# Optimization experiments

Measured on AMD Instinct MI355X. Metric: run time of the kernel, lower is better.

## Reference

```python
import jax, jax.numpy as jnp
import numpy as np

N_NODES = 2048
N_EDGES = 32768
N_GRAPH = 64
D_INJ = 240
D_EMB = 480
D_FEAT = 512
H = 4
DH = 120
SH_DIM = 9
N_RBF = 128
CUTOFF = 5.0
AVG_DEGREE = 16.0
AVG_NUM_NODES = 32.0
N_ITER = 2
MAX_ATOM = 64


def _ln(x):
    mu = jnp.mean(x, axis=-1, keepdims=True)
    var = jnp.var(x, axis=-1, keepdims=True)
    return (x - mu) * jax.lax.rsqrt(var + 1e-6)


def _sph(u):
    # component-normalized real spherical harmonics l=0,1,2 of unit vectors u [E,3]
    x, y, z = u[:, 0], u[:, 1], u[:, 2]
    s3 = np.sqrt(3.0); s15 = np.sqrt(15.0); s5 = np.sqrt(5.0)
    return jnp.stack([
        jnp.ones_like(x),
        s3 * x, s3 * y, s3 * z,
        s15 * x * y, s15 * y * z,
        0.5 * s5 * (3.0 * z * z - 1.0),
        s15 * x * z, 0.5 * s15 * (x * x - y * y)], axis=-1)


def _block(z, esrc, edst, sh, rbf, Wq, Wk, Wv, Wsh, Wr, Wo, F1, F2, res_ffn):
    # equivariant-style dot-product attention: gather -> edge compute -> segment softmax -> scatter
    x = _ln(z)
    q = (x @ Wq)[edst].reshape(-1, H, DH)
    k = (x @ Wk)[esrc].reshape(-1, H, DH)
    v = (x @ Wv)[esrc].reshape(-1, H, DH)
    m = (sh @ Wsh).reshape(-1, H, DH)          # SH tensor-product message modulation
    r = jax.nn.silu(rbf @ Wr)[:, :, None]      # radial gate per head [E,H,1]
    k = (k + m) * r
    v = (v + m) * r
    logit = jnp.sum(q * k, axis=-1) / np.sqrt(DH)   # [E,H]
    mx = jax.ops.segment_max(logit, edst, num_segments=N_NODES)
    mx = jnp.where(jnp.isfinite(mx), mx, 0.0)
    ex = jnp.exp(logit - mx[edst])
    den = jax.ops.segment_sum(ex, edst, num_segments=N_NODES)
    alpha = ex / (den[edst] + 1e-9)
    agg = jax.ops.segment_sum(alpha[:, :, None] * v, edst, num_segments=N_NODES)
    y = z + agg.reshape(N_NODES, H * DH) @ Wo
    out = jax.nn.silu(_ln(y) @ F1) @ F2
    return y + out if res_ffn else out


def _forward(pos, atom_table, degWr, degWsh,
             b0_Wq, b0_Wk, b0_Wv, b0_Wsh, b0_Wr, b0_Wo, b0_F1, b0_F2,
             bm_Wq, bm_Wk, bm_Wv, bm_Wsh, bm_Wr, bm_Wo, bm_F1, bm_F2,
             bf_Wq, bf_Wk, bf_Wv, bf_Wsh, bf_Wr, bf_Wo, bf_F1, bf_F2,
             hW1, hW2, node_atom, edge_src, edge_dst, batch):
    # ---- encode ----
    vec = pos[edge_src] - pos[edge_dst]
    d = jnp.sqrt(jnp.sum(vec * vec, axis=-1) + 1e-12)
    sh = _sph(vec / d[:, None])                              # [E,9]
    centers = jnp.linspace(0.0, CUTOFF, N_RBF)
    width = CUTOFF / N_RBF
    rbf = jnp.exp(-0.5 * jnp.square((d[:, None] - centers) / width))  # [E,128]
    atom = atom_table[node_atom]                             # [N,240]
    rad = jax.nn.silu(rbf @ degWr)                           # [E,9]
    deg = jax.ops.segment_sum((sh * rad) @ degWsh, edge_dst, num_segments=N_NODES) / AVG_DEGREE
    inj = atom + deg                                         # input-injection features
    # ---- DEQ fixed-point (unrolled) ----
    z = jnp.zeros((N_NODES, D_EMB), dtype=pos.dtype)
    for _ in range(N_ITER):
        z = _block(jnp.concatenate([z, inj], axis=-1), edge_src, edge_dst, sh, rbf,
                   b0_Wq, b0_Wk, b0_Wv, b0_Wsh, b0_Wr, b0_Wo, b0_F1, b0_F2, False)
        for i in range(4):
            z = _block(z, edge_src, edge_dst, sh, rbf,
                       bm_Wq[i], bm_Wk[i], bm_Wv[i], bm_Wsh[i], bm_Wr[i],
                       bm_Wo[i], bm_F1[i], bm_F2[i], True)
    # ---- decode ----
    feat = _block(z, edge_src, edge_dst, sh, rbf,
                  bf_Wq, bf_Wk, bf_Wv, bf_Wsh, bf_Wr, bf_Wo, bf_F1, bf_F2, False)
    feat = _ln(feat)
    e_node = jax.nn.silu(feat @ hW1) @ hW2                   # [N,1]
    return jax.ops.segment_sum(e_node, batch, num_segments=N_GRAPH) / np.sqrt(AVG_NUM_NODES)


def setup_inputs() -> dict:
    key = jax.random.key(0)
    it = iter(jax.random.split(key, 40))
    def nrm(shape):
        fan = shape[-2] if len(shape) >= 2 else shape[-1]
        return jax.random.normal(next(it), shape, jnp.float32) / np.sqrt(fan)
    inp = {}
    inp['pos'] = jax.random.normal(next(it), (N_NODES, 3), jnp.float32) * 2.0
    inp['node_atom'] = jax.random.randint(next(it), (N_NODES,), 0, MAX_ATOM)
    inp['edge_src'] = jax.random.randint(next(it), (N_EDGES,), 0, N_NODES)
    inp['edge_dst'] = jax.random.randint(next(it), (N_EDGES,), 0, N_NODES)
    inp['batch'] = jnp.sort(jax.random.randint(next(it), (N_NODES,), 0, N_GRAPH))
    inp['atom_table'] = nrm((MAX_ATOM, D_INJ))
    inp['degWr'] = nrm((N_RBF, SH_DIM))
    inp['degWsh'] = nrm((SH_DIM, D_INJ))
    DZ = D_EMB + D_INJ
    inp['b0_Wq'] = nrm((DZ, H * DH)); inp['b0_Wk'] = nrm((DZ, H * DH)); inp['b0_Wv'] = nrm((DZ, H * DH))
    inp['b0_Wsh'] = nrm((SH_DIM, H * DH)); inp['b0_Wr'] = nrm((N_RBF, H))
    inp['b0_Wo'] = nrm((H * DH, DZ)); inp['b0_F1'] = nrm((DZ, D_EMB)); inp['b0_F2'] = nrm((D_EMB, D_EMB))
    inp['bm_Wq'] = nrm((4, D_EMB, H * DH)); inp['bm_Wk'] = nrm((4, D_EMB, H * DH)); inp['bm_Wv'] = nrm((4, D_EMB, H * DH))
    inp['bm_Wsh'] = nrm((4, SH_DIM, H * DH)); inp['bm_Wr'] = nrm((4, N_RBF, H))
    inp['bm_Wo'] = nrm((4, H * DH, D_EMB)); inp['bm_F1'] = nrm((4, D_EMB, D_EMB)); inp['bm_F2'] = nrm((4, D_EMB, D_EMB))
    inp['bf_Wq'] = nrm((D_EMB, H * DH)); inp['bf_Wk'] = nrm((D_EMB, H * DH)); inp['bf_Wv'] = nrm((D_EMB, H * DH))
    inp['bf_Wsh'] = nrm((SH_DIM, H * DH)); inp['bf_Wr'] = nrm((N_RBF, H))
    inp['bf_Wo'] = nrm((H * DH, D_EMB)); inp['bf_F1'] = nrm((D_EMB, D_EMB)); inp['bf_F2'] = nrm((D_EMB, D_FEAT))
    inp['hW1'] = nrm((D_FEAT, D_FEAT)); inp['hW2'] = nrm((D_FEAT, 1))
    return inp


def reference(pos, atom_table, degWr, degWsh,
              b0_Wq, b0_Wk, b0_Wv, b0_Wsh, b0_Wr, b0_Wo, b0_F1, b0_F2,
              bm_Wq, bm_Wk, bm_Wv, bm_Wsh, bm_Wr, bm_Wo, bm_F1, bm_F2,
              bf_Wq, bf_Wk, bf_Wv, bf_Wsh, bf_Wr, bf_Wo, bf_F1, bf_F2,
              hW1, hW2, node_atom, edge_src, edge_dst, batch):
    return _forward(pos, atom_table, degWr, degWsh,
                    b0_Wq, b0_Wk, b0_Wv, b0_Wsh, b0_Wr, b0_Wo, b0_F1, b0_F2,
                    bm_Wq, bm_Wk, bm_Wv, bm_Wsh, bm_Wr, bm_Wo, bm_F1, bm_F2,
                    bf_Wq, bf_Wk, bf_Wv, bf_Wsh, bf_Wr, bf_Wo, bf_F1, bf_F2,
                    hW1, hW2, node_atom, edge_src, edge_dst, batch)
```

## Files before the change

### kernel.cpp

```cpp
#include <hip/hip_runtime.h>

#define NN 2048
#define NE 32768
#define NG 64
#define DINJ 240
#define DEMB 480
#define DFEAT 512
#define MAXDEG 192

typedef unsigned short ushort_t;
typedef __attribute__((ext_vector_type(8))) short short8;
typedef __attribute__((ext_vector_type(4))) float floatx4;

__device__ __forceinline__ float b2f(ushort_t u){
  union { unsigned u; float f; } x; x.u = ((unsigned)u) << 16; return x.f;
}
__device__ __forceinline__ ushort_t f2b(float f){
  union { float f; unsigned u; } x; x.f = f;
  unsigned r = x.u + 0x7FFFu + ((x.u >> 16) & 1u);
  return (ushort_t)(r >> 16);
}
__device__ __forceinline__ float wredsum(float v){
  #pragma unroll
  for (int o = 32; o > 0; o >>= 1) v += __shfl_xor(v, o, 64);
  return v;
}
__device__ __forceinline__ float silu_f(float x){ return x / (1.f + __expf(-x)); }

__global__ void zero_f32(float* p, int n){
  int i = blockIdx.x*256 + threadIdx.x; if (i < n) p[i] = 0.f;
}

__global__ void detect_kernel(const ushort_t* __restrict__ probe, int* flag){
  __shared__ int c;
  if (threadIdx.x == 0) c = 0;
  __syncthreads();
  ushort_t u = probe[2*threadIdx.x];
  int e = (u >> 7) & 0xFF;
  int plausible = (u == 0) || (e >= 100 && e <= 140);
  atomicAdd(&c, plausible);
  __syncthreads();
  if (threadIdx.x == 0) *flag = (c >= 192) ? 0 : 1;
}

struct CDesc { const void* src; float* dst; int n; };
struct CDescArr { CDesc d[11]; };
__global__ __launch_bounds__(256) void convert_inputs(CDescArr ca, const int* __restrict__ flag){
  CDesc cd = ca.d[blockIdx.y];
  int isf32 = *flag;
  for (int i = blockIdx.x*256 + threadIdx.x; i < cd.n; i += gridDim.x*256){
    cd.dst[i] = isf32 ? ((const float*)cd.src)[i] : b2f(((const ushort_t*)cd.src)[i]);
  }
}

struct TDesc { const void* src; ushort_t* dh; ushort_t* dl; int K; int M; int Kpad; int Mpad; int eoff; };
struct TDescArr { TDesc d[37]; };
__global__ __launch_bounds__(256) void transpose_all(TDescArr ta, const int* __restrict__ flag){
  TDesc td = ta.d[blockIdx.z];
  int k0 = blockIdx.x*32, m0 = blockIdx.y*32;
  if (k0 >= td.Kpad || m0 >= td.Mpad) return;
  int isf32 = *flag;
  __shared__ float lds[32*33];
  int tx = threadIdx.x & 31, ty = threadIdx.x >> 5;
  #pragma unroll
  for (int r = 0; r < 4; ++r){
    int kl = ty + r*8;
    int k = k0 + kl, mm = m0 + tx;
    float x = 0.f;
    if (k < td.K && mm < td.M){
      size_t si = (size_t)td.eoff + (size_t)k*td.M + mm;
      x = isf32 ? ((const float*)td.src)[si] : b2f(((const ushort_t*)td.src)[si]);
    }
    lds[kl*33 + tx] = x;
  }
  __syncthreads();
  #pragma unroll
  for (int r = 0; r < 4; ++r){
    int nl = ty + r*8;
    int n = m0 + nl, k = k0 + tx;
    if (n < td.Mpad && k < td.Kpad){
      float x = lds[tx*33 + nl];
      ushort_t h = f2b(x);
      size_t di = (size_t)n*td.Kpad + k;
      td.dh[di] = h;
      td.dl[di] = f2b(x - b2f(h));
    }
  }
}

__global__ void pack_wr(const float* __restrict__ b0Wr, const float* __restrict__ bmWr,
                        const float* __restrict__ bfWr, float* __restrict__ Wr_all){
  int idx = blockIdx.x*256 + threadIdx.x; if (idx >= 128*24) return;
  int k = idx / 24, o = idx - k*24;
  int slot = o >> 2, h = o & 3;
  const float* Wr = (slot == 0) ? b0Wr : ((slot <= 4) ? bmWr + (size_t)(slot-1)*512 : bfWr);
  Wr_all[idx] = Wr[k*4+h];
}

__global__ __launch_bounds__(128) void edge_all_kernel(
    const float* __restrict__ pos,
    const int* __restrict__ esrc, const int* __restrict__ edst,
    const float* __restrict__ degWr, const float* __restrict__ Wr_all,
    float* __restrict__ sh_out, float* __restrict__ t9,
    float* __restrict__ r_all){
  __shared__ float w9L[128*9];
  __shared__ float w24L[128*24];
  int t = threadIdx.x;
  for (int i = t; i < 128*9; i += 128)  w9L[i]  = degWr[i];
  for (int i = t; i < 128*24; i += 128) w24L[i] = Wr_all[i];
  __syncthreads();
  int e = blockIdx.x*128 + t; if (e >= NE) return;
  int s = esrc[e], d = edst[e];
  float x = pos[s*3+0] - pos[d*3+0];
  float y = pos[s*3+1] - pos[d*3+1];
  float z = pos[s*3+2] - pos[d*3+2];
  float dd = sqrtf(x*x + y*y + z*z + 1e-12f);
  float ix = x/dd, iy = y/dd, iz = z/dd;
  const float s3 = 1.7320508075688772f, s15 = 3.872983346207417f, s5 = 2.23606797749979f;
  float sh[9];
  sh[0] = 1.f; sh[1] = s3*ix; sh[2] = s3*iy; sh[3] = s3*iz;
  sh[4] = s15*ix*iy; sh[5] = s15*iy*iz; sh[6] = 0.5f*s5*(3.f*iz*iz - 1.f);
  sh[7] = s15*ix*iz; sh[8] = 0.5f*s15*(ix*ix - iy*iy);
  #pragma unroll
  for (int j = 0; j < 9; ++j) sh_out[(size_t)e*9+j] = sh[j];
  float t9a[9], ga[24];
  #pragma unroll
  for (int j = 0; j < 9; ++j) t9a[j] = 0.f;
  #pragma unroll
  for (int o = 0; o < 24; ++o) ga[o] = 0.f;
  for (int k = 0; k < 128; ++k){
    float c = (float)k * (5.0f/127.0f);
    float u = (dd - c) * (128.0f/5.0f);
    float rb = __expf(-0.5f*u*u);
    const float* w9  = w9L + k*9;
    const float* w24 = w24L + k*24;
    #pragma unroll
    for (int j = 0; j < 9; ++j) t9a[j] += rb*w9[j];
    #pragma unroll
    for (int o = 0; o < 24; ++o) ga[o] += rb*w24[o];
  }
  #pragma unroll
  for (int j = 0; j < 9; ++j) t9[(size_t)e*9+j] = sh[j]*silu_f(t9a[j]);
  #pragma unroll
  for (int o = 0; o < 24; ++o){
    int slot = o >> 2, h = o & 3;
    r_all[((size_t)slot*NE + e)*4 + h] = silu_f(ga[o]);
  }
}

__global__ void hist_kernel(const int* __restrict__ edst, int* counts){
  int e = blockIdx.x*256 + threadIdx.x; if (e < NE) atomicAdd(&counts[edst[e]], 1);
}
__global__ __launch_bounds__(1024) void scan_kernel(const int* __restrict__ counts,
                                                    int* rowptr, int* cursor){
  __shared__ int s[1024];
  int t = threadIdx.x;
  int c0 = counts[2*t], c1 = counts[2*t+1];
  s[t] = c0 + c1;
  __syncthreads();
  for (int off = 1; off < 1024; off <<= 1){
    int v = (t >= off) ? s[t-off] : 0;
    __syncthreads();
    s[t] += v;
    __syncthreads();
  }
  int excl = s[t] - (c0 + c1);
  rowptr[2*t]   = excl;       cursor[2*t]   = excl;
  rowptr[2*t+1] = excl + c0;  cursor[2*t+1] = excl + c0;
  if (t == 1023) rowptr[2048] = s[1023];
}
__global__ void scatter_kernel(const int* __restrict__ edst, int* cursor, int* perm){
  int e = blockIdx.x*256 + threadIdx.x; if (e >= NE) return;
  int p = atomicAdd(&cursor[edst[e]], 1);
  perm[p] = e;
}

__global__ __launch_bounds__(64) void inj_kernel(const float* __restrict__ t9,
    const int* __restrict__ rowptr, const int* __restrict__ perm,
    const int* __restrict__ node_atom, const float* __restrict__ atom_table,
    const float* __restrict__ degWsh, float* __restrict__ inj){
  int i = blockIdx.x; int lane = threadIdx.x;
  int b = rowptr[i], e = rowptr[i+1];
  float T[9];
  #pragma unroll
  for (int j = 0; j < 9; ++j) T[j] = 0.f;
  for (int idx = b; idx < e; ++idx){
    int ed = perm[idx];
    #pragma unroll
    for (int j = 0; j < 9; ++j) T[j] += t9[(size_t)ed*9+j];
  }
  int a = node_atom[i];
  for (int c = lane; c < DINJ; c += 64){
    float s = 0.f;
    #pragma unroll
    for (int j = 0; j < 9; ++j) s += T[j]*degWsh[j*DINJ+c];
    inj[(size_t)i*DINJ+c] = atom_table[(size_t)a*DINJ+c] + s*(1.0f/16.0f);
  }
}

__global__ __launch_bounds__(256) void ln_kernel(const float* __restrict__ in, int D,
                                                 int Kpad, ushort_t* __restrict__ oh){
  int i = blockIdx.x*4 + (threadIdx.x >> 6);
  int lane = threadIdx.x & 63;
  const float* row = in + (size_t)i*D;
  float s = 0.f, sq = 0.f;
  for (int d = lane; d < D; d += 64){ float x = row[d]; s += x; sq += x*x; }
  s = wredsum(s); sq = wredsum(sq);
  float mu = s / (float)D;
  float var = fmaxf(sq / (float)D - mu*mu, 0.f);
  float rs = rsqrtf(var + 1e-6f);
  ushort_t* ohrow = oh + (size_t)i*Kpad;
  for (int d = lane; d < D; d += 64) ohrow[d] = f2b((row[d]-mu)*rs);
  for (int d = D + lane; d < Kpad; d += 64) ohrow[d] = 0;
}

__global__ __launch_bounds__(256) void ln_cat_kernel(const float* __restrict__ z,
    const float* __restrict__ inj, ushort_t* __restrict__ oh){
  int i = blockIdx.x*4 + (threadIdx.x >> 6);
  int lane = threadIdx.x & 63;
  const float* zr = z + (size_t)i*480;
  const float* ir = inj + (size_t)i*240;
  float s = 0.f, sq = 0.f;
  for (int d = lane; d < 720; d += 64){
    float x = (d < 480) ? zr[d] : ir[d-480];
    s += x; sq += x*x;
  }
  s = wredsum(s); sq = wredsum(sq);
  float mu = s * (1.0f/720.0f);
  float var = fmaxf(sq * (1.0f/720.0f) - mu*mu, 0.f);
  float rs = rsqrtf(var + 1e-6f);
  ushort_t* ohrow = oh + (size_t)i*736;
  for (int d = lane; d < 720; d += 64){
    float x = (d < 480) ? zr[d] : ir[d-480];
    ohrow[d] = f2b((x-mu)*rs);
  }
  for (int d = 720 + lane; d < 736; d += 64) ohrow[d] = 0;
}

template<int KPAD, bool SPLITB>
__global__ __launch_bounds__(256) void gemm_bt(
    const ushort_t* __restrict__ A,
    const ushort_t* __restrict__ BTh, const ushort_t* __restrict__ BTl,
    int N, int ldc,
    float* __restrict__ Cf, ushort_t* __restrict__ Cb,
    const float* __restrict__ R, const float* __restrict__ R2, int flags){
  int lane = threadIdx.x & 63, wave = threadIdx.x >> 6;
  int row0 = blockIdx.y*64 + (wave>>1)*32;
  int col0 = blockIdx.x*64 + (wave&1)*32;
  int m = lane & 15, q4 = lane >> 4;
  size_t a0 = (size_t)(row0+m)*KPAD + q4*8;
  size_t a1 = a0 + (size_t)16*KPAD;
  size_t b0 = (size_t)(col0+m)*KPAD + q4*8;
  size_t b1 = b0 + (size_t)16*KPAD;
  floatx4 acc00 = {0,0,0,0}, acc01 = {0,0,0,0}, acc10 = {0,0,0,0}, acc11 = {0,0,0,0};
  constexpr int steps = KPAD >> 5;
  constexpr int DEPTH = SPLITB ? 3 : 4;
  struct Frag { short8 A0, A1, B0h, B1h, B0l, B1l; };
  auto loadF = [&](int s) -> Frag {
    Frag f;
    size_t o = (size_t)s*32;
    f.A0  = *(const short8*)(A   + a0 + o);
    f.A1  = *(const short8*)(A   + a1 + o);
    f.B0h = *(const short8*)(BTh + b0 + o);
    f.B1h = *(const short8*)(BTh + b1 + o);
    if (SPLITB){
      f.B0l = *(const short8*)(BTl + b0 + o);
      f.B1l = *(const short8*)(BTl + b1 + o);
    }
    return f;
  };
  Frag ring[DEPTH];
  #pragma unroll
  for (int d = 0; d < DEPTH; ++d) ring[d] = loadF(d < steps ? d : steps-1);
  #pragma unroll
  for (int s = 0; s < steps; ++s){
    Frag cur = ring[s % DEPTH];
    if (s + DEPTH < steps) ring[s % DEPTH] = loadF(s + DEPTH);
    acc00 = __builtin_amdgcn_mfma_f32_16x16x32_bf16(cur.A0, cur.B0h, acc00, 0, 0, 0);
    acc01 = __builtin_amdgcn_mfma_f32_16x16x32_bf16(cur.A0, cur.B1h, acc01, 0, 0, 0);
    acc10 = __builtin_amdgcn_mfma_f32_16x16x32_bf16(cur.A1, cur.B0h, acc10, 0, 0, 0);
    acc11 = __builtin_amdgcn_mfma_f32_16x16x32_bf16(cur.A1, cur.B1h, acc11, 0, 0, 0);
    if (SPLITB){
      acc00 = __builtin_amdgcn_mfma_f32_16x16x32_bf16(cur.A0, cur.B0l, acc00, 0, 0, 0);
      acc01 = __builtin_amdgcn_mfma_f32_16x16x32_bf16(cur.A0, cur.B1l, acc01, 0, 0, 0);
      acc10 = __builtin_amdgcn_mfma_f32_16x16x32_bf16(cur.A1, cur.B0l, acc10, 0, 0, 0);
      acc11 = __builtin_amdgcn_mfma_f32_16x16x32_bf16(cur.A1, cur.B1l, acc11, 0, 0, 0);
    }
  }
  #pragma unroll
  for (int rr = 0; rr < 2; ++rr){
    #pragma unroll
    for (int cc = 0; cc < 2; ++cc){
      int col = col0 + cc*16 + m;
      if (col >= N) continue;
      floatx4 acc = rr ? (cc ? acc11 : acc10) : (cc ? acc01 : acc00);
      int rowb = row0 + rr*16 + q4*4;
      #pragma unroll
      for (int r = 0; r < 4; ++r){
        int row = rowb + r;
        size_t idx = (size_t)row*ldc + col;
        float v = acc[r];
        if (flags & 2){
          if (flags & 8)
            v += (col < 480) ? R[(size_t)row*480 + col] : R2[(size_t)row*240 + (col-480)];
          else
            v += R[idx];
        }
        if (flags & 1) v = silu_f(v);
        if (flags & 4) Cb[idx] = f2b(v);
        else           Cf[idx] = v;
      }
    }
  }
}

__global__ __launch_bounds__(256) void node_attn_kernel(
    const float* __restrict__ qkv, const float* __restrict__ sh,
    const float* __restrict__ Wsh, const float* __restrict__ r_slot,
    const int* __restrict__ rowptr, const int* __restrict__ perm,
    const int* __restrict__ esrc, ushort_t* __restrict__ aggh){
  int i = blockIdx.x; int t = threadIdx.x;
  int lane = t & 63, w = t >> 6;
  int b = rowptr[i]; int deg = min(rowptr[i+1] - b, MAXDEG);
  __shared__ float qL[480];
  __shared__ float PqL[36];
  __shared__ float logitL[MAXDEG*4];
  __shared__ float rL[MAXDEG*4];
  __shared__ int eL[MAXDEG], srcL[MAXDEG];
  __shared__ float S[36];
  __shared__ float mxs[4], dens[4];
  for (int d = t; d < 480; d += 256) qL[d] = qkv[(size_t)i*1440 + d];
  for (int idx = t; idx < deg; idx += 256){
    int e = perm[b+idx];
    eL[idx] = e;
    srcL[idx] = esrc[e];
  }
  __syncthreads();
  if (t < 36){
    int h = t/9, j = t - h*9;
    const float* ws = Wsh + (size_t)j*DEMB + h*120;
    const float* qh = qL + h*120;
    float p = 0.f;
    for (int k = 0; k < 120; ++k) p += qh[k]*ws[k];
    PqL[t] = p;
  }
  __syncthreads();
  const float inv = 0.091287092917527686f;
  for (int base = 0; base < deg; base += 64){
    int idx = base + (t >> 2);
    if (idx < deg){
      int h = t & 3;
      int e = eL[idx], s = srcL[idx];
      const float4* kk = (const float4*)(qkv + (size_t)s*1440 + 480 + h*120);
      const float4* qq = (const float4*)(qL + h*120);
      float p = 0.f;
      #pragma unroll
      for (int it = 0; it < 30; ++it){
        float4 a = qq[it], bb = kk[it];
        p += a.x*bb.x + a.y*bb.y + a.z*bb.z + a.w*bb.w;
      }
      float mmq = 0.f;
      const float* she = sh + (size_t)e*9;
      #pragma unroll
      for (int j = 0; j < 9; ++j) mmq += she[j]*PqL[h*9+j];
      float rr = r_slot[(size_t)e*4+h];
      rL[idx*4+h] = rr;
      logitL[idx*4+h] = rr*(p + mmq)*inv;
    }
  }
  __syncthreads();
  float mx = -1e30f;
  for (int idx = lane; idx < deg; idx += 64) mx = fmaxf(mx, logitL[idx*4+w]);
  #pragma unroll
  for (int o = 32; o > 0; o >>= 1) mx = fmaxf(mx, __shfl_xor(mx, o, 64));
  if (deg == 0) mx = 0.f;
  float den = 0.f;
  for (int idx = lane; idx < deg; idx += 64) den += __expf(logitL[idx*4+w]-mx);
  den = wredsum(den) + 1e-9f;
  if (lane == 0){ mxs[w] = mx; dens[w] = den; }
  __syncthreads();
  for (int j = t; j < deg*4; j += 256){
    int h = j & 3;
    logitL[j] = __expf(logitL[j]-mxs[h]) / dens[h] * rL[j];
  }
  __syncthreads();
  float a0 = 0.f, a1 = 0.f;
  int d0 = 2*t, h2 = d0/120;
  if (t >= 240){
    for (int o = t - 240; o < 36; o += 16){
      int h = o/9, j = o - h*9;
      float a = 0.f;
      for (int idx = 0; idx < deg; ++idx)
        a += logitL[idx*4+h]*sh[(size_t)eL[idx]*9+j];
      S[o] = a;
    }
  } else {
    for (int idx = 0; idx < deg; ++idx){
      float wgt = logitL[idx*4+h2];
      float2 vv = *(const float2*)(qkv + (size_t)srcL[idx]*1440 + 960 + d0);
      a0 += wgt*vv.x; a1 += wgt*vv.y;
    }
  }
  __syncthreads();
  if (t < 240){
    float mm0 = 0.f, mm1 = 0.f;
    #pragma unroll
    for (int j = 0; j < 9; ++j){
      mm0 += S[h2*9+j]*Wsh[j*DEMB + d0];
      mm1 += S[h2*9+j]*Wsh[j*DEMB + d0 + 1];
    }
    aggh[(size_t)i*DEMB + d0]     = f2b(a0 + mm0);
    aggh[(size_t)i*DEMB + d0 + 1] = f2b(a1 + mm1);
  }
}

__global__ __launch_bounds__(256) void head_dot_kernel(const ushort_t* __restrict__ g1h,
    const float* __restrict__ hW2, const int* __restrict__ batch, float* gsum){
  int i = blockIdx.x*4 + (threadIdx.x >> 6);
  int lane = threadIdx.x & 63;
  float s = 0.f;
  for (int d = lane; d < DFEAT; d += 64)
    s += b2f(g1h[(size_t)i*DFEAT + d]) * hW2[d];
  s = wredsum(s);
  if (lane == 0) atomicAdd(&gsum[batch[i]], s);
}
__global__ void finalize_kernel(const float* __restrict__ gsum,
                                const int* __restrict__ flag, void* out){
  int g = threadIdx.x;
  if (g < NG){
    float v = gsum[g] * 0.17677669529663687f;
    if (*flag) ((float*)out)[g] = v;
    else       ((ushort_t*)out)[g] = f2b(v);
  }
}

extern "C" void kernel_launch(void* const* d_in, const int* in_sizes, int n_in,
                              void* d_out, int out_size, void* d_ws, size_t ws_size,
                              hipStream_t stream) {
  (void)in_sizes; (void)n_in; (void)out_size; (void)ws_size;
  const void* pos        = d_in[0];
  const int*  node_atom  = (const int*)d_in[1];
  const int*  esrc       = (const int*)d_in[2];
  const int*  edst       = (const int*)d_in[3];
  const int*  batch      = (const int*)d_in[4];
  const void* atom_table = d_in[5];
  const void* degWr      = d_in[6];
  const void* degWsh     = d_in[7];
  const void* b0_Wq  = d_in[8];
  const void* b0_Wk  = d_in[9];
  const void* b0_Wv  = d_in[10];
  const void* b0_Wsh = d_in[11];
  const void* b0_Wr  = d_in[12];
  const void* b0_Wo  = d_in[13];
  const void* b0_F1  = d_in[14];
  const void* b0_F2  = d_in[15];
  const void* bm_Wq  = d_in[16];
  const void* bm_Wk  = d_in[17];
  const void* bm_Wv  = d_in[18];
  const void* bm_Wsh = d_in[19];
  const void* bm_Wr  = d_in[20];
  const void* bm_Wo  = d_in[21];
  const void* bm_F1  = d_in[22];
  const void* bm_F2  = d_in[23];
  const void* bf_Wq  = d_in[24];
  const void* bf_Wk  = d_in[25];
  const void* bf_Wv  = d_in[26];
  const void* bf_Wsh = d_in[27];
  const void* bf_Wr  = d_in[28];
  const void* bf_Wo  = d_in[29];
  const void* bf_F1  = d_in[30];
  const void* bf_F2  = d_in[31];
  const void* hW1    = d_in[32];
  const void* hW2    = d_in[33];

  char* bws = (char*)d_ws;
  size_t off = 0;
  auto alloc = [&](size_t bytes) -> void* {
    void* p = bws + off;
    off += (bytes + 255) & ~(size_t)255;
    return p;
  };
  int* dflag   = (int*)alloc(256);
  float* sh_f  = (float*)alloc((size_t)NE*9*4);
  float* t9    = (float*)alloc((size_t)NE*9*4);
  int* counts  = (int*)alloc(2048*4);
  int* rowptr  = (int*)alloc(2049*4);
  int* cursor  = (int*)alloc(2048*4);
  int* perm    = (int*)alloc((size_t)NE*4);
  float* injb  = (float*)alloc((size_t)NN*DINJ*4);
  float* zA    = (float*)alloc((size_t)NN*512*4);
  float* zB    = (float*)alloc((size_t)NN*512*4);
  ushort_t* xlnh = (ushort_t*)alloc((size_t)NN*736*2);
  float* qkvb  = (float*)alloc((size_t)NN*1440*4);
  float* Wr_all = (float*)alloc((size_t)128*24*4);
  float* r_all = (float*)alloc((size_t)6*NE*4*4);
  ushort_t* aggh = (ushort_t*)alloc((size_t)NN*DEMB*2);
  float* ybuf  = (float*)alloc((size_t)NN*720*4);
  ushort_t* h1h = (ushort_t*)alloc((size_t)NN*DEMB*2);
  ushort_t* g1h = (ushort_t*)alloc((size_t)NN*DFEAT*2);
  float* gsum  = (float*)alloc(64*4);

  float* pos_c    = (float*)alloc((size_t)NN*3*4);
  float* atom_c   = (float*)alloc((size_t)64*DINJ*4);
  float* degWr_c  = (float*)alloc((size_t)128*9*4);
  float* degWsh_c = (float*)alloc((size_t)9*DINJ*4);
  float* b0_Wsh_c = (float*)alloc((size_t)9*480*4);
  float* b0_Wr_c  = (float*)alloc((size_t)128*4*4);
  float* bm_Wsh_c = (float*)alloc((size_t)4*9*480*4);
  float* bm_Wr_c  = (float*)alloc((size_t)4*128*4*4);
  float* bf_Wsh_c = (float*)alloc((size_t)9*480*4);
  float* bf_Wr_c  = (float*)alloc((size_t)128*4*4);
  float* hW2_c    = (float*)alloc((size_t)512*4);

  auto allocW = [&](size_t elems, ushort_t*& h, ushort_t*& l){
    h = (ushort_t*)alloc(elems*2); l = (ushort_t*)alloc(elems*2);
  };
  ushort_t *b0_qkvTh,*b0_qkvTl,*b0_WoTh,*b0_WoTl,*b0_F1Th,*b0_F1Tl,*b0_F2Th,*b0_F2Tl;
  allocW((size_t)1472*736, b0_qkvTh, b0_qkvTl);
  allocW((size_t)768*480,  b0_WoTh,  b0_WoTl);
  allocW((size_t)512*736,  b0_F1Th,  b0_F1Tl);
  allocW((size_t)512*480,  b0_F2Th,  b0_F2Tl);
  ushort_t *bm_qkvTh[4],*bm_qkvTl[4],*bm_WoTh[4],*bm_WoTl[4],*bm_F1Th[4],*bm_F1Tl[4],*bm_F2Th[4],*bm_F2Tl[4];
  for (int i = 0; i < 4; ++i){
    allocW((size_t)1472*480, bm_qkvTh[i], bm_qkvTl[i]);
    allocW((size_t)512*480,  bm_WoTh[i],  bm_WoTl[i]);
    allocW((size_t)512*480,  bm_F1Th[i],  bm_F1Tl[i]);
    allocW((size_t)512*480,  bm_F2Th[i],  bm_F2Tl[i]);
  }
  ushort_t *bf_qkvTh,*bf_qkvTl,*bf_WoTh,*bf_WoTl,*bf_F1Th,*bf_F1Tl,*bf_F2Th,*bf_F2Tl,*hW1Th,*hW1Tl;
  allocW((size_t)1472*480, bf_qkvTh, bf_qkvTl);
  allocW((size_t)512*480,  bf_WoTh,  bf_WoTl);
  allocW((size_t)512*480,  bf_F1Th,  bf_F1Tl);
  allocW((size_t)512*480,  bf_F2Th,  bf_F2Tl);
  allocW((size_t)512*512,  hW1Th,    hW1Tl);

  detect_kernel<<<1, 256, 0, stream>>>((const ushort_t*)atom_table, dflag);

  CDescArr ca;
  int ci = 0;
  auto addC = [&](const void* s, float* d, int n){
    ca.d[ci].src = s; ca.d[ci].dst = d; ca.d[ci].n = n; ++ci;
  };
  addC(pos, pos_c, NN*3);
  addC(atom_table, atom_c, 64*DINJ);
  addC(degWr, degWr_c, 128*9);
  addC(degWsh, degWsh_c, 9*DINJ);
  addC(b0_Wsh, b0_Wsh_c, 9*480);
  addC(b0_Wr, b0_Wr_c, 128*4);
  addC(bm_Wsh, bm_Wsh_c, 4*9*480);
  addC(bm_Wr, bm_Wr_c, 4*128*4);
  addC(bf_Wsh, bf_Wsh_c, 9*480);
  addC(bf_Wr, bf_Wr_c, 128*4);
  addC(hW2, hW2_c, 512);
  convert_inputs<<<dim3(8, 11), 256, 0, stream>>>(ca, dflag);

  TDescArr ta;
  int ti = 0;
  auto addT = [&](const void* s, ushort_t* dh, ushort_t* dl, int K, int M,
                  int Kp, int Mp, int rowoff, int eo){
    ta.d[ti].src = s;
    ta.d[ti].dh = dh + (size_t)rowoff*Kp;
    ta.d[ti].dl = dl + (size_t)rowoff*Kp;
    ta.d[ti].K = K; ta.d[ti].M = M; ta.d[ti].Kpad = Kp; ta.d[ti].Mpad = Mp;
    ta.d[ti].eoff = eo; ++ti;
  };
  addT(b0_Wq, b0_qkvTh, b0_qkvTl, 720, 480, 736, 480, 0,   0);
  addT(b0_Wk, b0_qkvTh, b0_qkvTl, 720, 480, 736, 480, 480, 0);
  addT(b0_Wv, b0_qkvTh, b0_qkvTl, 720, 480, 736, 512, 960, 0);
  addT(b0_Wo, b0_WoTh,  b0_WoTl,  480, 720, 480, 768, 0,   0);
  addT(b0_F1, b0_F1Th,  b0_F1Tl,  720, 480, 736, 512, 0,   0);
  addT(b0_F2, b0_F2Th,  b0_F2Tl,  480, 480, 480, 512, 0,   0);
  for (int i = 0; i < 4; ++i){
    int eo = i*480*480;
    addT(bm_Wq, bm_qkvTh[i], bm_qkvTl[i], 480, 480, 480, 480, 0,   eo);
    addT(bm_Wk, bm_qkvTh[i], bm_qkvTl[i], 480, 480, 480, 480, 480, eo);
    addT(bm_Wv, bm_qkvTh[i], bm_qkvTl[i], 480, 480, 480, 512, 960, eo);
    addT(bm_Wo, bm_WoTh[i],  bm_WoTl[i],  480, 480, 480, 512, 0,   eo);
    addT(bm_F1, bm_F1Th[i],  bm_F1Tl[i],  480, 480, 480, 512, 0,   eo);
    addT(bm_F2, bm_F2Th[i],  bm_F2Tl[i],  480, 480, 480, 512, 0,   eo);
  }
  addT(bf_Wq, bf_qkvTh, bf_qkvTl, 480, 480, 480, 480, 0,   0);
  addT(bf_Wk, bf_qkvTh, bf_qkvTl, 480, 480, 480, 480, 480, 0);
  addT(bf_Wv, bf_qkvTh, bf_qkvTl, 480, 480, 480, 512, 960, 0);
  addT(bf_Wo, bf_WoTh,  bf_WoTl,  480, 480, 480, 512, 0,   0);
  addT(bf_F1, bf_F1Th,  bf_F1Tl,  480, 480, 480, 512, 0,   0);
  addT(bf_F2, bf_F2Th,  bf_F2Tl,  480, 512, 480, 512, 0,   0);
  addT(hW1,   hW1Th,    hW1Tl,    512, 512, 512, 512, 0,   0);
  transpose_all<<<dim3(23, 24, 37), 256, 0, stream>>>(ta, dflag);

  pack_wr<<<12, 256, 0, stream>>>(b0_Wr_c, bm_Wr_c, bf_Wr_c, Wr_all);
  edge_all_kernel<<<NE/128, 128, 0, stream>>>(pos_c, esrc, edst, degWr_c, Wr_all,
                                              sh_f, t9, r_all);

  zero_f32<<<(2048 + 255)/256, 256, 0, stream>>>((float*)counts, 2048);
  hist_kernel<<<NE/256, 256, 0, stream>>>(edst, counts);
  scan_kernel<<<1, 1024, 0, stream>>>(counts, rowptr, cursor);
  scatter_kernel<<<NE/256, 256, 0, stream>>>(edst, cursor, perm);

  inj_kernel<<<NN, 64, 0, stream>>>(t9, rowptr, perm, node_atom, atom_c, degWsh_c, injb);
  zero_f32<<<(NN*DEMB)/256, 256, 0, stream>>>(zA, NN*DEMB);

  auto gemm = [&](const ushort_t* A, const ushort_t* BTh, const ushort_t* BTl,
                  int N, int Npad, int Kp, int ldc,
                  float* Cf, ushort_t* Cb, const float* R, const float* R2,
                  int flags, bool split){
    dim3 g(Npad/64, 32);
    if (split){
      if (Kp == 480)
        gemm_bt<480,true><<<g, 256, 0, stream>>>(A, BTh, BTl, N, ldc, Cf, Cb, R, R2, flags);
      else if (Kp == 512)
        gemm_bt<512,true><<<g, 256, 0, stream>>>(A, BTh, BTl, N, ldc, Cf, Cb, R, R2, flags);
      else
        gemm_bt<736,true><<<g, 256, 0, stream>>>(A, BTh, BTl, N, ldc, Cf, Cb, R, R2, flags);
    } else {
      if (Kp == 480)
        gemm_bt<480,false><<<g, 256, 0, stream>>>(A, BTh, BTl, N, ldc, Cf, Cb, R, R2, flags);
      else if (Kp == 512)
        gemm_bt<512,false><<<g, 256, 0, stream>>>(A, BTh, BTl, N, ldc, Cf, Cb, R, R2, flags);
      else
        gemm_bt<736,false><<<g, 256, 0, stream>>>(A, BTh, BTl, N, ldc, Cf, Cb, R, R2, flags);
    }
  };

  struct BW {
    const float *Wsh, *r_slot;
    const ushort_t *qkvTh,*qkvTl,*WoTh,*WoTl,*F1Th,*F1Tl,*F2Th,*F2Tl;
    int Din, Kpad, Dout; bool res;
  };
  auto run_block = [&](const BW& bw, const float* zin, const float* zinj, float* zout){
    if (zinj) ln_cat_kernel<<<NN/4, 256, 0, stream>>>(zin, zinj, xlnh);
    else      ln_kernel<<<NN/4, 256, 0, stream>>>(zin, bw.Din, bw.Kpad, xlnh);
    gemm(xlnh, bw.qkvTh, bw.qkvTl, 1440, 1472, bw.Kpad, 1440,
         qkvb, nullptr, nullptr, nullptr, 0, true);
    node_attn_kernel<<<NN, 256, 0, stream>>>(qkvb, sh_f, bw.Wsh, bw.r_slot,
                                             rowptr, perm, esrc, aggh);
    int WoNpad = (bw.Din == 720) ? 768 : 512;
    gemm(aggh, bw.WoTh, bw.WoTl, bw.Din, WoNpad, 480, bw.Din,
         ybuf, nullptr, zin, zinj, zinj ? (2|8) : 2, false);
    ln_kernel<<<NN/4, 256, 0, stream>>>(ybuf, bw.Din, bw.Kpad, xlnh);
    gemm(xlnh, bw.F1Th, bw.F1Tl, DEMB, 512, bw.Kpad, DEMB,
         nullptr, h1h, nullptr, nullptr, 1|4, false);
    gemm(h1h, bw.F2Th, bw.F2Tl, bw.Dout, 512, 480, bw.Dout,
         zout, nullptr, bw.res ? ybuf : nullptr, nullptr, bw.res ? 2 : 0, false);
  };

  BW b0 = { b0_Wsh_c, r_all + (size_t)0*NE*4,
            b0_qkvTh,b0_qkvTl,b0_WoTh,b0_WoTl,b0_F1Th,b0_F1Tl,b0_F2Th,b0_F2Tl,
            720, 736, 480, false };
  BW bm[4];
  for (int i = 0; i < 4; ++i){
    bm[i] = { bm_Wsh_c + (size_t)i*9*480, r_all + (size_t)(1+i)*NE*4,
              bm_qkvTh[i],bm_qkvTl[i],bm_WoTh[i],bm_WoTl[i],
              bm_F1Th[i],bm_F1Tl[i],bm_F2Th[i],bm_F2Tl[i],
              480, 480, 480, true };
  }
  BW bf = { bf_Wsh_c, r_all + (size_t)5*NE*4,
            bf_qkvTh,bf_qkvTl,bf_WoTh,bf_WoTl,bf_F1Th,bf_F1Tl,bf_F2Th,bf_F2Tl,
            480, 480, 512, false };

  float* z  = zA;
  float* z2 = zB;
  for (int iter = 0; iter < 2; ++iter){
    run_block(b0, z, injb, z2);
    { float* tmp = z; z = z2; z2 = tmp; }
    for (int i = 0; i < 4; ++i){
      run_block(bm[i], z, nullptr, z2);
      { float* tmp = z; z = z2; z2 = tmp; }
    }
  }
  run_block(bf, z, nullptr, z2);
  ln_kernel<<<NN/4, 256, 0, stream>>>(z2, DFEAT, DFEAT, xlnh);
  gemm(xlnh, hW1Th, hW1Tl, DFEAT, 512, DFEAT, DFEAT,
       nullptr, g1h, nullptr, nullptr, 1|4, true);
  zero_f32<<<1, 64, 0, stream>>>(gsum, 64);
  head_dot_kernel<<<NN/4, 256, 0, stream>>>(g1h, hW2_c, batch, gsum);
  finalize_kernel<<<1, 64, 0, stream>>>(gsum, dflag, d_out);
}
```

Baseline: 1.393 ms.

## Fuse LayerNorm into GEMM prologue using per-row stats emitted by producer GEMM epilogues

Removes the standalone LayerNorm kernels. Producer GEMMs (Wo, F2) now write per-row partial sums and sums of squares into a stats buffer from their epilogue, and inj_kernel does the same for the injection features. Consumer GEMMs read fp32 activations, rebuild mean and variance from these partials, and normalise and pack to bf16 on the fly while loading A fragments. This saves a kernel launch and a bf16 round-trip per LayerNorm. In exchange the A loads are fp32 with extra ALU work, the stats use the less stable one-pass variance, and the bf16 packing now truncates instead of rounding.

```diff
diff --git a/kernel.cpp b/kernel.cpp
--- a/kernel.cpp
+++ b/kernel.cpp
@@ -19,6 +19,9 @@
   union { float f; unsigned u; } x; x.f = f;
   unsigned r = x.u + 0x7FFFu + ((x.u >> 16) & 1u);
   return (ushort_t)(r >> 16);
+}
+__device__ __forceinline__ unsigned pk2(float a, float b){
+  return (__float_as_uint(a) >> 16) | (__float_as_uint(b) & 0xFFFF0000u);
 }
 __device__ __forceinline__ float wredsum(float v){
   #pragma unroll
@@ -178,7 +181,8 @@
 __global__ __launch_bounds__(64) void inj_kernel(const float* __restrict__ t9,
     const int* __restrict__ rowptr, const int* __restrict__ perm,
     const int* __restrict__ node_atom, const float* __restrict__ atom_table,
-    const float* __restrict__ degWsh, float* __restrict__ inj){
+    const float* __restrict__ degWsh, float* __restrict__ inj,
+    float* __restrict__ injS){
   int i = blockIdx.x; int lane = threadIdx.x;
   int b = rowptr[i], e = rowptr[i+1];
   float T[9];
@@ -190,68 +194,113 @@
     for (int j = 0; j < 9; ++j) T[j] += t9[(size_t)ed*9+j];
   }
   int a = node_atom[i];
+  float ps = 0.f, pq = 0.f;
   for (int c = lane; c < DINJ; c += 64){
     float s = 0.f;
     #pragma unroll
     for (int j = 0; j < 9; ++j) s += T[j]*degWsh[j*DINJ+c];
-    inj[(size_t)i*DINJ+c] = atom_table[(size_t)a*DINJ+c] + s*(1.0f/16.0f);
-  }
-}
-
-__global__ __launch_bounds__(256) void ln_kernel(const float* __restrict__ in, int D,
-                                                 int Kpad, ushort_t* __restrict__ oh){
-  int i = blockIdx.x*4 + (threadIdx.x >> 6);
-  int lane = threadIdx.x & 63;
-  const float* row = in + (size_t)i*D;
-  float s = 0.f, sq = 0.f;
-  for (int d = lane; d < D; d += 64){ float x = row[d]; s += x; sq += x*x; }
-  s = wredsum(s); sq = wredsum(sq);
-  float mu = s / (float)D;
-  float var = fmaxf(sq / (float)D - mu*mu, 0.f);
-  float rs = rsqrtf(var + 1e-6f);
-  ushort_t* ohrow = oh + (size_t)i*Kpad;
-  for (int d = lane; d < D; d += 64) ohrow[d] = f2b((row[d]-mu)*rs);
-  for (int d = D + lane; d < Kpad; d += 64) ohrow[d] = 0;
-}
-
-__global__ __launch_bounds__(256) void ln_cat_kernel(const float* __restrict__ z,
-    const float* __restrict__ inj, ushort_t* __restrict__ oh){
-  int i = blockIdx.x*4 + (threadIdx.x >> 6);
-  int lane = threadIdx.x & 63;
-  const float* zr = z + (size_t)i*480;
-  const float* ir = inj + (size_t)i*240;
-  float s = 0.f, sq = 0.f;
-  for (int d = lane; d < 720; d += 64){
-    float x = (d < 480) ? zr[d] : ir[d-480];
-    s += x; sq += x*x;
-  }
-  s = wredsum(s); sq = wredsum(sq);
-  float mu = s * (1.0f/720.0f);
-  float var = fmaxf(sq * (1.0f/720.0f) - mu*mu, 0.f);
-  float rs = rsqrtf(var + 1e-6f);
-  ushort_t* ohrow = oh + (size_t)i*736;
-  for (int d = lane; d < 720; d += 64){
-    float x = (d < 480) ? zr[d] : ir[d-480];
-    ohrow[d] = f2b((x-mu)*rs);
-  }
-  for (int d = 720 + lane; d < 736; d += 64) ohrow[d] = 0;
-}
-
-template<int KPAD, bool SPLITB>
+    float v = atom_table[(size_t)a*DINJ+c] + s*(1.0f/16.0f);
+    inj[(size_t)i*DINJ+c] = v;
+    ps += v; pq += v*v;
+  }
+  ps = wredsum(ps); pq = wredsum(pq);
+  if (lane == 0){ injS[i*2] = ps; injS[i*2+1] = pq; }
+}
+
+template<int KPAD, bool SPLITB, int LNA, bool STATS>
 __global__ __launch_bounds__(256) void gemm_bt(
-    const ushort_t* __restrict__ A,
+    const void* __restrict__ Abuf, const float* __restrict__ Ainj,
+    const float* __restrict__ injS,
+    const float* __restrict__ stIn, int stInStride, int nslots, int Din,
     const ushort_t* __restrict__ BTh, const ushort_t* __restrict__ BTl,
     int N, int ldc,
     float* __restrict__ Cf, ushort_t* __restrict__ Cb,
-    const float* __restrict__ R, const float* __restrict__ R2, int flags){
+    const float* __restrict__ R, const float* __restrict__ R2,
+    float* __restrict__ stOut, int stOutStride, int flags){
   int lane = threadIdx.x & 63, wave = threadIdx.x >> 6;
   int row0 = blockIdx.y*64 + (wave>>1)*32;
   int col0 = blockIdx.x*64 + (wave&1)*32;
   int m = lane & 15, q4 = lane >> 4;
-  size_t a0 = (size_t)(row0+m)*KPAD + q4*8;
-  size_t a1 = a0 + (size_t)16*KPAD;
   size_t b0 = (size_t)(col0+m)*KPAD + q4*8;
   size_t b1 = b0 + (size_t)16*KPAD;
+  int r0 = row0 + m, r1 = row0 + 16 + m;
+  const ushort_t* A16 = (const ushort_t*)Abuf;
+  const float*    A32 = (const float*)Abuf;
+  size_t a0 = 0, a1 = 0;
+  const float *az0 = nullptr, *az1 = nullptr, *aj0 = nullptr, *aj1 = nullptr;
+  float rs0 = 0.f, nm0 = 0.f, rs1 = 0.f, nm1 = 0.f;
+  if constexpr (LNA == 0){
+    a0 = (size_t)r0*KPAD + q4*8;
+    a1 = (size_t)r1*KPAD + q4*8;
+  } else {
+    int zw = (LNA == 2) ? 480 : Din;
+    az0 = A32 + (size_t)r0*zw;
+    az1 = A32 + (size_t)r1*zw;
+    if constexpr (LNA == 2){
+      aj0 = Ainj + (size_t)r0*240;
+      aj1 = Ainj + (size_t)r1*240;
+    }
+    float DD = (LNA == 2) ? 720.f : (float)Din;
+    #pragma unroll
+    for (int which = 0; which < 2; ++which){
+      int row = which ? r1 : r0;
+      float s = 0.f, q = 0.f;
+      const float* st = stIn + (size_t)row*stInStride;
+      for (int t2 = 0; t2 < nslots; ++t2){ s += st[2*t2]; q += st[2*t2+1]; }
+      if constexpr (LNA == 2){ s += injS[row*2]; q += injS[row*2+1]; }
+      float mu = s / DD;
+      float var = fmaxf(q / DD - mu*mu, 0.f);
+      float rs = rsqrtf(var + 1e-6f);
+      float nm = -mu*rs;
+      if (which){ rs1 = rs; nm1 = nm; } else { rs0 = rs; nm0 = nm; }
+    }
+  }
+  auto loadAfrag = [&](int s, int which) -> short8 {
+    if constexpr (LNA == 0){
+      size_t base = which ? a1 : a0;
+      return *(const short8*)(A16 + base + (size_t)s*32);
+    } else {
+      int k = q4*8 + s*32;
+      float x[8];
+      const float* az = which ? az1 : az0;
+      bool zero = false;
+      if constexpr (LNA == 1){
+        if (k < Din){
+          float4 p = *(const float4*)(az + k);
+          float4 q2 = *(const float4*)(az + k + 4);
+          x[0]=p.x; x[1]=p.y; x[2]=p.z; x[3]=p.w;
+          x[4]=q2.x; x[5]=q2.y; x[6]=q2.z; x[7]=q2.w;
+        } else zero = true;
+      } else {
+        if (k < 480){
+          float4 p = *(const float4*)(az + k);
+          float4 q2 = *(const float4*)(az + k + 4);
+          x[0]=p.x; x[1]=p.y; x[2]=p.z; x[3]=p.w;
+          x[4]=q2.x; x[5]=q2.y; x[6]=q2.z; x[7]=q2.w;
+        } else if (k < 720){
+          const float* aj = which ? aj1 : aj0;
+          float4 p = *(const float4*)(aj + (k - 480));
+          float4 q2 = *(const float4*)(aj + (k - 480) + 4);
+          x[0]=p.x; x[1]=p.y; x[2]=p.z; x[3]=p.w;
+          x[4]=q2.x; x[5]=q2.y; x[6]=q2.z; x[7]=q2.w;
+        } else zero = true;
+      }
+      union { short8 v; unsigned u[4]; } o;
+      if (zero){
+        o.u[0] = o.u[1] = o.u[2] = o.u[3] = 0u;
+      } else {
+        float rs = which ? rs1 : rs0;
+        float nm = which ? nm1 : nm0;
+        #pragma unroll
+        for (int p2 = 0; p2 < 4; ++p2){
+          float f0 = fmaf(x[2*p2],   rs, nm);
+          float f1 = fmaf(x[2*p2+1], rs, nm);
+          o.u[p2] = pk2(f0, f1);
+        }
+      }
+      return o.v;
+    }
+  };
   floatx4 acc00 = {0,0,0,0}, acc01 = {0,0,0,0}, acc10 = {0,0,0,0}, acc11 = {0,0,0,0};
   constexpr int steps = KPAD >> 5;
   constexpr int DEPTH = SPLITB ? 3 : 4;
@@ -259,8 +308,8 @@
   auto loadF = [&](int s) -> Frag {
     Frag f;
     size_t o = (size_t)s*32;
-    f.A0  = *(const short8*)(A   + a0 + o);
-    f.A1  = *(const short8*)(A   + a1 + o);
+    f.A0  = loadAfrag(s, 0);
+    f.A1  = loadAfrag(s, 1);
     f.B0h = *(const short8*)(BTh + b0 + o);
     f.B1h = *(const short8*)(BTh + b1 + o);
     if (SPLITB){
@@ -287,28 +336,54 @@
       acc11 = __builtin_amdgcn_mfma_f32_16x16x32_bf16(cur.A1, cur.B1l, acc11, 0, 0, 0);
     }
   }
+  float vf[2][2][4];
   #pragma unroll
   for (int rr = 0; rr < 2; ++rr){
     #pragma unroll
     for (int cc = 0; cc < 2; ++cc){
       int col = col0 + cc*16 + m;
-      if (col >= N) continue;
+      bool cv = (col < N);
       floatx4 acc = rr ? (cc ? acc11 : acc10) : (cc ? acc01 : acc00);
       int rowb = row0 + rr*16 + q4*4;
       #pragma unroll
       for (int r = 0; r < 4; ++r){
-        int row = rowb + r;
-        size_t idx = (size_t)row*ldc + col;
-        float v = acc[r];
-        if (flags & 2){
-          if (flags & 8)
-            v += (col < 480) ? R[(size_t)row*480 + col] : R2[(size_t)row*240 + (col-480)];
-          else
-            v += R[idx];
+        float v = 0.f;
+        if (cv){
+          int row = rowb + r;
+          size_t idx = (size_t)row*ldc + col;
+          v = acc[r];
+          if (flags & 2){
+            if (flags & 8)
+              v += (col < 480) ? R[(size_t)row*480 + col] : R2[(size_t)row*240 + (col-480)];
+            else
+              v += R[idx];
+          }
+          if (flags & 1) v = silu_f(v);
+          if (flags & 4) Cb[idx] = f2b(v);
+          else           Cf[idx] = v;
         }
-        if (flags & 1) v = silu_f(v);
-        if (flags & 4) Cb[idx] = f2b(v);
-        else           Cf[idx] = v;
+        vf[rr][cc][r] = v;
+      }
+    }
+  }
+  if constexpr (STATS){
+    int slot = blockIdx.x*2 + (wave & 1);
+    #pragma unroll
+    for (int rr = 0; rr < 2; ++rr){
+      #pragma unroll
+      for (int r = 0; r < 4; ++r){
+        float sm = vf[rr][0][r] + vf[rr][1][r];
+        float sq = vf[rr][0][r]*vf[rr][0][r] + vf[rr][1][r]*vf[rr][1][r];
+        #pragma unroll
+        for (int o2 = 1; o2 < 16; o2 <<= 1){
+          sm += __shfl_xor(sm, o2, 64);
+          sq += __shfl_xor(sq, o2, 64);
+        }
+        if (m == 0){
+          int row = row0 + rr*16 + q4*4 + r;
+          stOut[(size_t)row*stOutStride + slot*2]     = sm;
+          stOut[(size_t)row*stOutStride + slot*2 + 1] = sq;
+        }
       }
     }
   }
@@ -488,9 +563,12 @@
   int* cursor  = (int*)alloc(2048*4);
   int* perm    = (int*)alloc((size_t)NE*4);
   float* injb  = (float*)alloc((size_t)NN*DINJ*4);
+  float* injS  = (float*)alloc((size_t)NN*2*4);
   float* zA    = (float*)alloc((size_t)NN*512*4);
+  float* stZA  = (float*)alloc((size_t)NN*32*4);
   float* zB    = (float*)alloc((size_t)NN*512*4);
-  ushort_t* xlnh = (ushort_t*)alloc((size_t)NN*736*2);
+  float* stZB  = (float*)alloc((size_t)NN*32*4);
+  float* stY   = (float*)alloc((size_t)NN*48*4);
   float* qkvb  = (float*)alloc((size_t)NN*1440*4);
   float* Wr_all = (float*)alloc((size_t)128*24*4);
   float* r_all = (float*)alloc((size_t)6*NE*4*4);
@@ -597,81 +675,81 @@
   scan_kernel<<<1, 1024, 0, stream>>>(counts, rowptr, cursor);
   scatter_kernel<<<NE/256, 256, 0, stream>>>(edst, cursor, perm);
 
-  inj_kernel<<<NN, 64, 0, stream>>>(t9, rowptr, perm, node_atom, atom_c, degWsh_c, injb);
-  zero_f32<<<(NN*DEMB)/256, 256, 0, stream>>>(zA, NN*DEMB);
-
-  auto gemm = [&](const ushort_t* A, const ushort_t* BTh, const ushort_t* BTl,
-                  int N, int Npad, int Kp, int ldc,
-                  float* Cf, ushort_t* Cb, const float* R, const float* R2,
-                  int flags, bool split){
-    dim3 g(Npad/64, 32);
-    if (split){
-      if (Kp == 480)
-        gemm_bt<480,true><<<g, 256, 0, stream>>>(A, BTh, BTl, N, ldc, Cf, Cb, R, R2, flags);
-      else if (Kp == 512)
-        gemm_bt<512,true><<<g, 256, 0, stream>>>(A, BTh, BTl, N, ldc, Cf, Cb, R, R2, flags);
-      else
-        gemm_bt<736,true><<<g, 256, 0, stream>>>(A, BTh, BTl, N, ldc, Cf, Cb, R, R2, flags);
-    } else {
-      if (Kp == 480)
-        gemm_bt<480,false><<<g, 256, 0, stream>>>(A, BTh, BTl, N, ldc, Cf, Cb, R, R2, flags);
-      else if (Kp == 512)
-        gemm_bt<512,false><<<g, 256, 0, stream>>>(A, BTh, BTl, N, ldc, Cf, Cb, R, R2, flags);
-      else
-        gemm_bt<736,false><<<g, 256, 0, stream>>>(A, BTh, BTl, N, ldc, Cf, Cb, R, R2, flags);
-    }
-  };
+  inj_kernel<<<NN, 64, 0, stream>>>(t9, rowptr, perm, node_atom, atom_c, degWsh_c,
+                                    injb, injS);
+  zero_f32<<<(NN*544 + 255)/256, 256, 0, stream>>>(zA, NN*544);
 
   struct BW {
     const float *Wsh, *r_slot;
     const ushort_t *qkvTh,*qkvTl,*WoTh,*WoTl,*F1Th,*F1Tl,*F2Th,*F2Tl;
-    int Din, Kpad, Dout; bool res;
+    int Din, Dout; bool res;
   };
-  auto run_block = [&](const BW& bw, const float* zin, const float* zinj, float* zout){
-    if (zinj) ln_cat_kernel<<<NN/4, 256, 0, stream>>>(zin, zinj, xlnh);
-    else      ln_kernel<<<NN/4, 256, 0, stream>>>(zin, bw.Din, bw.Kpad, xlnh);
-    gemm(xlnh, bw.qkvTh, bw.qkvTl, 1440, 1472, bw.Kpad, 1440,
-         qkvb, nullptr, nullptr, nullptr, 0, true);
+  auto run_block = [&](const BW& bw, const float* zin, float* zinStats,
+                       const float* zinj, float* zout, float* zoutStats){
+    if (zinj){
+      gemm_bt<736,true,2,false><<<dim3(23,32), 256, 0, stream>>>(
+        zin, zinj, injS, zinStats, 32, 16, 720,
+        bw.qkvTh, bw.qkvTl, 1440, 1440, qkvb, nullptr,
+        nullptr, nullptr, nullptr, 0, 0);
+    } else {
+      gemm_bt<480,true,1,false><<<dim3(23,32), 256, 0, stream>>>(
+        zin, nullptr, nullptr, zinStats, 32, 16, 480,
+        bw.qkvTh, bw.qkvTl, 1440, 1440, qkvb, nullptr,
+        nullptr, nullptr, nullptr, 0, 0);
+    }
     node_attn_kernel<<<NN, 256, 0, stream>>>(qkvb, sh_f, bw.Wsh, bw.r_slot,
                                              rowptr, perm, esrc, aggh);
     int WoNpad = (bw.Din == 720) ? 768 : 512;
-    gemm(aggh, bw.WoTh, bw.WoTl, bw.Din, WoNpad, 480, bw.Din,
-         ybuf, nullptr, zin, zinj, zinj ? (2|8) : 2, false);
-    ln_kernel<<<NN/4, 256, 0, stream>>>(ybuf, bw.Din, bw.Kpad, xlnh);
-    gemm(xlnh, bw.F1Th, bw.F1Tl, DEMB, 512, bw.Kpad, DEMB,
-         nullptr, h1h, nullptr, nullptr, 1|4, false);
-    gemm(h1h, bw.F2Th, bw.F2Tl, bw.Dout, 512, 480, bw.Dout,
-         zout, nullptr, bw.res ? ybuf : nullptr, nullptr, bw.res ? 2 : 0, false);
+    gemm_bt<480,false,0,true><<<dim3(WoNpad/64,32), 256, 0, stream>>>(
+      aggh, nullptr, nullptr, nullptr, 0, 0, 0,
+      bw.WoTh, bw.WoTl, bw.Din, bw.Din, ybuf, nullptr,
+      zin, zinj, stY, 48, zinj ? (2|8) : 2);
+    if (bw.Din == 720){
+      gemm_bt<736,false,1,false><<<dim3(8,32), 256, 0, stream>>>(
+        ybuf, nullptr, nullptr, stY, 48, 24, 720,
+        bw.F1Th, bw.F1Tl, 480, 480, nullptr, h1h,
+        nullptr, nullptr, nullptr, 0, 1|4);
+    } else {
+      gemm_bt<480,false,1,false><<<dim3(8,32), 256, 0, stream>>>(
+        ybuf, nullptr, nullptr, stY, 48, 16, 480,
+        bw.F1Th, bw.F1Tl, 480, 480, nullptr, h1h,
+        nullptr, nullptr, nullptr, 0, 1|4);
+    }
+    gemm_bt<480,false,0,true><<<dim3(8,32), 256, 0, stream>>>(
+      h1h, nullptr, nullptr, nullptr, 0, 0, 0,
+      bw.F2Th, bw.F2Tl, bw.Dout, bw.Dout, zout, nullptr,
+      bw.res ? ybuf : nullptr, nullptr, zoutStats, 32, bw.res ? 2 : 0);
   };
 
   BW b0 = { b0_Wsh_c, r_all + (size_t)0*NE*4,
             b0_qkvTh,b0_qkvTl,b0_WoTh,b0_WoTl,b0_F1Th,b0_F1Tl,b0_F2Th,b0_F2Tl,
-            720, 736, 480, false };
+            720, 480, false };
   BW bm[4];
   for (int i = 0; i < 4; ++i){
     bm[i] = { bm_Wsh_c + (size_t)i*9*480, r_all + (size_t)(1+i)*NE*4,
               bm_qkvTh[i],bm_qkvTl[i],bm_WoTh[i],bm_WoTl[i],
               bm_F1Th[i],bm_F1Tl[i],bm_F2Th[i],bm_F2Tl[i],
-              480, 480, 480, true };
+              480, 480, true };
   }
   BW bf = { bf_Wsh_c, r_all + (size_t)5*NE*4,
             bf_qkvTh,bf_qkvTl,bf_WoTh,bf_WoTl,bf_F1Th,bf_F1Tl,bf_F2Th,bf_F2Tl,
-            480, 480, 512, false };
-
-  float* z  = zA;
-  float* z2 = zB;
+            480, 512, false };
+
+  float* z  = zA;  float* zS  = stZA;
+  float* z2 = zB;  float* z2S = stZB;
   for (int iter = 0; iter < 2; ++iter){
-    run_block(b0, z, injb, z2);
-    { float* tmp = z; z = z2; z2 = tmp; }
+    run_block(b0, z, zS, injb, z2, z2S);
+    { float* t1 = z; z = z2; z2 = t1; float* t2 = zS; zS = z2S; z2S = t2; }
     for (int i = 0; i < 4; ++i){
-      run_block(bm[i], z, nullptr, z2);
-      { float* tmp = z; z = z2; z2 = tmp; }
-    }
-  }
-  run_block(bf, z, nullptr, z2);
-  ln_kernel<<<NN/4, 256, 0, stream>>>(z2, DFEAT, DFEAT, xlnh);
-  gemm(xlnh, hW1Th, hW1Tl, DFEAT, 512, DFEAT, DFEAT,
-       nullptr, g1h, nullptr, nullptr, 1|4, true);
+      run_block(bm[i], z, zS, nullptr, z2, z2S);
+      { float* t1 = z; z = z2; z2 = t1; float* t2 = zS; zS = z2S; z2S = t2; }
+    }
+  }
+  run_block(bf, z, zS, nullptr, z2, z2S);
+  gemm_bt<512,true,1,false><<<dim3(8,32), 256, 0, stream>>>(
+    z2, nullptr, nullptr, z2S, 32, 16, 512,
+    hW1Th, hW1Tl, 512, 512, nullptr, g1h,
+    nullptr, nullptr, nullptr, 0, 1|4);
   zero_f32<<<1, 64, 0, stream>>>(gsum, 64);
   head_dot_kernel<<<NN/4, 256, 0, stream>>>(g1h, hW2_c, batch, gsum);
   finalize_kernel<<<1, 64, 0, stream>>>(gsum, dflag, d_out);
```

Result: slower. 1.635 ms (+17.3%).
